# Optimization experiments

Measured on AMD Instinct MI355X. Metric: run time of the kernel, lower is better.

Reference implementation:

```python
import jax, jax.numpy as jnp
import numpy as np

K = 64        # top-k from init_kwargs
TAU = 1.0     # temperature at step=0: tau_start*(1-0) + tau_end*0


def setup_inputs() -> dict:
    key = jax.random.key(0)
    k1, k2 = jax.random.split(key)
    B, N = 2048, 8192
    logits = jax.random.normal(k1, (B, N), dtype=jnp.float32)
    # gumbels = -log(Exp(1)) == standard Gumbel noise
    gumbel_noise = jax.random.gumbel(k2, (B, N), dtype=jnp.float32)
    return {"logits": logits, "gumbel_noise": gumbel_noise}


def reference(logits, gumbel_noise):
    # training path of GumbelTopK (step=0 -> tau=TAU, hard=True)
    g = (logits + gumbel_noise) / TAU                       # [B, N]
    order = jnp.argsort(-g, axis=-1)                        # descending sort order
    sorted_g = jnp.take_along_axis(g, order, axis=-1)
    cumsum = jnp.cumsum(jax.nn.softmax(sorted_g, axis=-1), axis=-1)
    mask = (cumsum <= K).astype(sorted_g.dtype)             # NB: faithful to source (<= k)
    sorted_y = mask * jax.nn.softmax(sorted_g / TAU, axis=-1)
    # scatter back to original positions == gather by inverse permutation
    inv = jnp.argsort(order, axis=-1)
    y = jnp.take_along_axis(sorted_y, inv, axis=-1)         # [B, N]
    # hard straight-through: one-hot-k of y
    k = min(K, y.shape[-1])
    _, idx = jax.lax.top_k(y, k)                            # [B, k]
    rows = jnp.arange(y.shape[0])[:, None]
    y_hard = jnp.zeros_like(y).at[rows, idx].set(1.0)
    return jax.lax.stop_gradient(y_hard - y) + y
```

## Files before the change

kernel.cpp:

```cpp
#include <hip/hip_runtime.h>

constexpr int N = 8192;
constexpr int K = 64;
constexpr int THREADS = 512;
constexpr int WAVES = THREADS / 64;
constexpr int EPT = N / THREADS;
constexpr int VEC = EPT / 4;
constexpr int CAP = 1024;

constexpr float FTHRESH = 4.75f;

typedef float f32x4 __attribute__((ext_vector_type(4)));

__device__ __forceinline__ unsigned orderable(float f) {
    unsigned x = __float_as_uint(f);
    return (x & 0x80000000u) ? ~x : (x | 0x80000000u);
}

__device__ __forceinline__ void barrier_nd() {
    asm volatile("s_waitcnt lgkmcnt(0)" ::: "memory");
    __builtin_amdgcn_s_barrier();
    asm volatile("" ::: "memory");
}

__global__ __launch_bounds__(THREADS, 4)
void gumbel_topk_onehot(const float* __restrict__ logits,
                        const float* __restrict__ noise,
                        float* __restrict__ out)
{
    __shared__ __align__(16) unsigned hist[2048];
    __shared__ __align__(16) unsigned cand[CAP];
    __shared__ unsigned wavesum[WAVES];
    __shared__ unsigned ccount;
    __shared__ unsigned sel_bin, sel_kth, sel_cnt;
    __shared__ unsigned r_val, r_take, r_ceq;

    const int tid  = threadIdx.x;
    const int lane = tid & 63;
    const int wave = tid >> 6;
    const long long row = blockIdx.x;

    if (tid == 0) ccount = 0u;

    const f32x4* l4 = (const f32x4*)(logits + row * (long long)N);
    const f32x4* n4 = (const f32x4*)(noise  + row * (long long)N);
    f32x4 av[VEC], bv[VEC];
#pragma unroll
    for (int i = 0; i < VEC; ++i) av[i] = l4[tid + i * THREADS];
#pragma unroll
    for (int i = 0; i < VEC; ++i) bv[i] = n4[tid + i * THREADS];
#pragma unroll
    for (int i = 0; i < VEC; ++i)
        asm volatile("" : "+v"(av[i]), "+v"(bv[i]));

    float s[EPT];
#pragma unroll
    for (int i = 0; i < VEC; ++i) {
        s[4*i+0] = av[i].x + bv[i].x;
        s[4*i+1] = av[i].y + bv[i].y;
        s[4*i+2] = av[i].z + bv[i].z;
        s[4*i+3] = av[i].w + bv[i].w;
    }
    barrier_nd();

#pragma unroll
    for (int e = 0; e < EPT; ++e) {
        if (s[e] >= FTHRESH) {
            unsigned pos = atomicAdd(&ccount, 1u);
            if (pos < (unsigned)CAP) cand[pos] = __float_as_uint(s[e]);
        }
    }
    barrier_nd();

    const unsigned c = ccount;
    float Tf;
    unsigned take_eq, c_eq;

    if (c >= (unsigned)K && c <= (unsigned)THREADS) {
        const bool have = (tid < (int)c);
        const unsigned myv = have ? cand[tid] : 0u;
        if (tid < (int)((c + 63u) & ~63u)) {
            unsigned g = 0, eq = 0;
            int j = 0;
            for (; j + 4 <= (int)c; j += 4) {
                uint4 v = ((const uint4*)cand)[j >> 2];
                g  += (v.x >  myv) + (v.y >  myv) + (v.z >  myv) + (v.w >  myv);
                eq += (v.x == myv) + (v.y == myv) + (v.z == myv) + (v.w == myv);
            }
            for (; j < (int)c; ++j) {
                unsigned v = cand[j];
                g += (v > myv); eq += (v == myv);
            }
            if (have && g < (unsigned)K && g + eq >= (unsigned)K) {
                r_val  = myv;
                r_take = (unsigned)K - g;
                r_ceq  = eq;
            }
        }
        barrier_nd();
        Tf      = __uint_as_float(r_val);
        take_eq = r_take;
        c_eq    = r_ceq;
    } else {
        unsigned kth = K;

#define SELECT_BIN(BPT)                                                      \
        {                                                                    \
            unsigned p = 0;                                                  \
            _Pragma("unroll")                                                \
            for (int j = 0; j < (BPT); ++j) p += hist[tid * (BPT) + j];      \
            unsigned sc = p;                                                 \
            _Pragma("unroll")                                                \
            for (int off = 1; off < 64; off <<= 1) {                         \
                unsigned v = __shfl_down(sc, off);                           \
                if (lane + off < 64) sc += v;                                \
            }                                                                \
            if (lane == 0) wavesum[wave] = sc;                               \
            __syncthreads();                                                 \
            unsigned S = sc;                                                 \
            _Pragma("unroll")                                                \
            for (int w = 0; w < WAVES; ++w) if (w > wave) S += wavesum[w];   \
            unsigned Snext = S - p;                                          \
            if (S >= kth && Snext < kth) {                                   \
                unsigned cum = Snext;                                        \
                for (int j = (BPT) - 1; j >= 0; --j) {                       \
                    unsigned b = tid * (BPT) + j;                            \
                    unsigned cc = hist[b];                                   \
                    if (cum + cc >= kth) {                                   \
                        sel_bin = b;                                         \
                        sel_kth = kth - cum;                                 \
                        sel_cnt = cc;                                        \
                        break;                                               \
                    }                                                        \
                    cum += cc;                                               \
                }                                                            \
            }                                                                \
            __syncthreads();                                                 \
        }

        ((uint4*)hist)[tid] = make_uint4(0u, 0u, 0u, 0u);
        if (tid == 0) ccount = 0u;
        __syncthreads();
#pragma unroll
        for (int e = 0; e < EPT; ++e)
            atomicAdd(&hist[orderable(s[e]) >> 21], 1u);
        __syncthreads();
        SELECT_BIN(4)
        const unsigned b1   = sel_bin;
        const unsigned cnt1 = sel_cnt;
        kth = sel_kth;

#pragma unroll
        for (int e = 0; e < EPT; ++e) {
            unsigned k_e = orderable(s[e]);
            if ((k_e >> 21) == b1) {
                unsigned pos = atomicAdd(&ccount, 1u);
                if (pos < (unsigned)CAP) cand[pos] = k_e & 0x1FFFFFu;
            }
        }
        __syncthreads();
        const bool use_cand = (cnt1 <= (unsigned)CAP);

        ((uint4*)hist)[tid] = make_uint4(0u, 0u, 0u, 0u);
        __syncthreads();
        if (use_cand) {
            for (int i = tid; i < (int)cnt1; i += THREADS)
                atomicAdd(&hist[cand[i] >> 10], 1u);
        } else {
#pragma unroll
            for (int e = 0; e < EPT; ++e) {
                unsigned k_e = orderable(s[e]);
                if ((k_e >> 21) == b1)
                    atomicAdd(&hist[(k_e >> 10) & 0x7FFu], 1u);
            }
        }
        __syncthreads();
        SELECT_BIN(4)
        const unsigned b2 = sel_bin;
        kth = sel_kth;
        __syncthreads();

        if (tid < 256) ((uint4*)hist)[tid] = make_uint4(0u, 0u, 0u, 0u);
        __syncthreads();
        if (use_cand) {
            for (int i = tid; i < (int)cnt1; i += THREADS) {
                unsigned cv = cand[i];
                if ((cv >> 10) == b2) atomicAdd(&hist[cv & 0x3FFu], 1u);
            }
        } else {
            const unsigned pfx = (b1 << 11) | b2;
#pragma unroll
            for (int e = 0; e < EPT; ++e) {
                unsigned k_e = orderable(s[e]);
                if ((k_e >> 10) == pfx)
                    atomicAdd(&hist[k_e & 0x3FFu], 1u);
            }
        }
        __syncthreads();
        SELECT_BIN(2)
        const unsigned T_ord = (b1 << 21) | (b2 << 10) | sel_bin;
        const unsigned bits = (T_ord & 0x80000000u) ? (T_ord & 0x7FFFFFFFu)
                                                    : ~T_ord;
        Tf      = __uint_as_float(bits);
        take_eq = sel_kth;
        c_eq    = sel_cnt;
#undef SELECT_BIN
    }

    const bool fast = (take_eq == c_eq);

    f32x4* orow = (f32x4*)(out + row * (long long)N);
    if (fast) {
#pragma unroll
        for (int i = 0; i < VEC; ++i) {
            f32x4 o;
            o.x = (s[4*i+0] >= Tf) ? 1.0f : 0.0f;
            o.y = (s[4*i+1] >= Tf) ? 1.0f : 0.0f;
            o.z = (s[4*i+2] >= Tf) ? 1.0f : 0.0f;
            o.w = (s[4*i+3] >= Tf) ? 1.0f : 0.0f;
            __builtin_nontemporal_store(o, &orow[tid + i * THREADS]);
        }
    } else {
#pragma unroll
        for (int i = 0; i < VEC; ++i) {
            f32x4 o;
            o.x = (s[4*i+0] > Tf) ? 1.0f : 0.0f;
            o.y = (s[4*i+1] > Tf) ? 1.0f : 0.0f;
            o.z = (s[4*i+2] > Tf) ? 1.0f : 0.0f;
            o.w = (s[4*i+3] > Tf) ? 1.0f : 0.0f;
            __builtin_nontemporal_store(o, &orow[tid + i * THREADS]);
        }
        __syncthreads();
        if (tid == 0) {
            const float* lf = logits + row * (long long)N;
            const float* nf = noise  + row * (long long)N;
            float* of = out + row * (long long)N;
            unsigned cc = 0;
            for (int i = 0; i < N; ++i) {
                if (lf[i] + nf[i] == Tf) {
                    of[i] = 1.0f;
                    if (++cc == take_eq) break;
                }
            }
        }
    }
}

extern "C" void kernel_launch(void* const* d_in, const int* in_sizes, int n_in,
                              void* d_out, int out_size, void* d_ws, size_t ws_size,
                              hipStream_t stream) {
    const float* logits = (const float*)d_in[0];
    const float* noise  = (const float*)d_in[1];
    float* out = (float*)d_out;
    const int rows = in_sizes[0] / N;
    gumbel_topk_onehot<<<rows, THREADS, 0, stream>>>(logits, noise, out);
}
```

Before: 173.7 us.

## Halve block size, use per-wave ballot compaction instead of shared atomics

Drops the block to 256 threads, so each thread holds 32 elements and more blocks fit per CU. Candidates above the threshold are gathered with ballot and popcount into per-wave segments instead of atomics on one shared counter, and the rank-selection step reads from those segments. Global loads are interleaved in pairs, and nontemporal output stores become ordinary stores. The cost is more register pressure per thread and a fallback to the histogram path when any wave finds more than 64 candidates.

New measurement: 190.4 us. +9.6%, slower.

```diff
diff --git a/kernel.cpp b/kernel.cpp
--- a/kernel.cpp
+++ b/kernel.cpp
@@ -2,10 +2,11 @@
 
 constexpr int N = 8192;
 constexpr int K = 64;
-constexpr int THREADS = 512;
+constexpr int THREADS = 256;
 constexpr int WAVES = THREADS / 64;
 constexpr int EPT = N / THREADS;
 constexpr int VEC = EPT / 4;
+constexpr int SEGCAP = 64;
 constexpr int CAP = 1024;
 
 constexpr float FTHRESH = 4.75f;
@@ -23,13 +24,15 @@
     asm volatile("" ::: "memory");
 }
 
-__global__ __launch_bounds__(THREADS, 4)
+__global__ __launch_bounds__(THREADS, 8)
 void gumbel_topk_onehot(const float* __restrict__ logits,
                         const float* __restrict__ noise,
                         float* __restrict__ out)
 {
     __shared__ __align__(16) unsigned hist[2048];
     __shared__ __align__(16) unsigned cand[CAP];
+    __shared__ __align__(16) unsigned seg[WAVES][SEGCAP];
+    __shared__ unsigned scnt[WAVES];
     __shared__ unsigned wavesum[WAVES];
     __shared__ unsigned ccount;
     __shared__ unsigned sel_bin, sel_kth, sel_cnt;
@@ -40,56 +43,69 @@
     const int wave = tid >> 6;
     const long long row = blockIdx.x;
 
-    if (tid == 0) ccount = 0u;
-
     const f32x4* l4 = (const f32x4*)(logits + row * (long long)N);
     const f32x4* n4 = (const f32x4*)(noise  + row * (long long)N);
-    f32x4 av[VEC], bv[VEC];
-#pragma unroll
-    for (int i = 0; i < VEC; ++i) av[i] = l4[tid + i * THREADS];
-#pragma unroll
-    for (int i = 0; i < VEC; ++i) bv[i] = n4[tid + i * THREADS];
-#pragma unroll
-    for (int i = 0; i < VEC; ++i)
-        asm volatile("" : "+v"(av[i]), "+v"(bv[i]));
-
     float s[EPT];
 #pragma unroll
-    for (int i = 0; i < VEC; ++i) {
-        s[4*i+0] = av[i].x + bv[i].x;
-        s[4*i+1] = av[i].y + bv[i].y;
-        s[4*i+2] = av[i].z + bv[i].z;
-        s[4*i+3] = av[i].w + bv[i].w;
-    }
+    for (int g4 = 0; g4 < VEC; g4 += 2) {
+        f32x4 a0 = l4[tid + (g4 + 0) * THREADS];
+        f32x4 a1 = l4[tid + (g4 + 1) * THREADS];
+        f32x4 b0 = n4[tid + (g4 + 0) * THREADS];
+        f32x4 b1 = n4[tid + (g4 + 1) * THREADS];
+#pragma unroll
+        for (int e = 0; e < 4; ++e) s[4 * g4 + e]     = a0[e] + b0[e];
+#pragma unroll
+        for (int e = 0; e < 4; ++e) s[4 * g4 + 4 + e] = a1[e] + b1[e];
+    }
+
+    const unsigned long long below = (1ull << lane) - 1ull;
+    unsigned cw = 0;
+#pragma unroll
+    for (int e = 0; e < EPT; ++e) {
+        const bool p = (s[e] >= FTHRESH);
+        const unsigned long long m = __ballot(p);
+        if (p) {
+            const unsigned pos = cw + (unsigned)__popcll(m & below);
+            if (pos < (unsigned)SEGCAP) seg[wave][pos] = __float_as_uint(s[e]);
+        }
+        cw += (unsigned)__popcll(m);
+    }
+    if (lane == 0) scnt[wave] = cw;
     barrier_nd();
 
-#pragma unroll
-    for (int e = 0; e < EPT; ++e) {
-        if (s[e] >= FTHRESH) {
-            unsigned pos = atomicAdd(&ccount, 1u);
-            if (pos < (unsigned)CAP) cand[pos] = __float_as_uint(s[e]);
-        }
-    }
-    barrier_nd();
-
-    const unsigned c = ccount;
+    const unsigned c0 = scnt[0], c1 = scnt[1], c2 = scnt[2], c3 = scnt[3];
+    const unsigned c  = c0 + c1 + c2 + c3;
+    const unsigned mx = max(max(c0, c1), max(c2, c3));
+    const unsigned cws[WAVES] = {c0, c1, c2, c3};
+
     float Tf;
     unsigned take_eq, c_eq;
-
-    if (c >= (unsigned)K && c <= (unsigned)THREADS) {
+    bool fast;
+
+    if (c >= (unsigned)K && c <= (unsigned)THREADS && mx <= (unsigned)SEGCAP) {
         const bool have = (tid < (int)c);
-        const unsigned myv = have ? cand[tid] : 0u;
+        unsigned myv = 0u;
+        if (have) {
+            unsigned d = (unsigned)tid, w2 = 0;
+            if (d >= c0) { d -= c0; w2 = 1;
+                if (d >= c1) { d -= c1; w2 = 2;
+                    if (d >= c2) { d -= c2; w2 = 3; } } }
+            myv = seg[w2][d];
+        }
         if (tid < (int)((c + 63u) & ~63u)) {
             unsigned g = 0, eq = 0;
-            int j = 0;
-            for (; j + 4 <= (int)c; j += 4) {
-                uint4 v = ((const uint4*)cand)[j >> 2];
-                g  += (v.x >  myv) + (v.y >  myv) + (v.z >  myv) + (v.w >  myv);
-                eq += (v.x == myv) + (v.y == myv) + (v.z == myv) + (v.w == myv);
-            }
-            for (; j < (int)c; ++j) {
-                unsigned v = cand[j];
-                g += (v > myv); eq += (v == myv);
+#pragma unroll
+            for (int w2 = 0; w2 < WAVES; ++w2) {
+                const unsigned cn = cws[w2];
+                const uint4* s4 = (const uint4*)seg[w2];
+                for (unsigned q = 0; q * 4 < cn; ++q) {
+                    const uint4 v = s4[q];
+                    const unsigned i0 = q * 4;
+                    if (i0 + 0 < cn) { g += v.x > myv; eq += v.x == myv; }
+                    if (i0 + 1 < cn) { g += v.y > myv; eq += v.y == myv; }
+                    if (i0 + 2 < cn) { g += v.z > myv; eq += v.z == myv; }
+                    if (i0 + 3 < cn) { g += v.w > myv; eq += v.w == myv; }
+                }
             }
             if (have && g < (unsigned)K && g + eq >= (unsigned)K) {
                 r_val  = myv;
@@ -101,6 +117,7 @@
         Tf      = __uint_as_float(r_val);
         take_eq = r_take;
         c_eq    = r_ceq;
+        fast    = (take_eq == c_eq);
     } else {
         unsigned kth = K;
 
@@ -138,30 +155,32 @@
             __syncthreads();                                                 \
         }
 
-        ((uint4*)hist)[tid] = make_uint4(0u, 0u, 0u, 0u);
+        for (int i = tid; i < 512; i += THREADS)
+            ((uint4*)hist)[i] = make_uint4(0u, 0u, 0u, 0u);
         if (tid == 0) ccount = 0u;
         __syncthreads();
 #pragma unroll
         for (int e = 0; e < EPT; ++e)
             atomicAdd(&hist[orderable(s[e]) >> 21], 1u);
         __syncthreads();
-        SELECT_BIN(4)
+        SELECT_BIN(8)
         const unsigned b1   = sel_bin;
         const unsigned cnt1 = sel_cnt;
         kth = sel_kth;
 
 #pragma unroll
         for (int e = 0; e < EPT; ++e) {
-            unsigned k_e = orderable(s[e]);
+            const unsigned k_e = orderable(s[e]);
             if ((k_e >> 21) == b1) {
-                unsigned pos = atomicAdd(&ccount, 1u);
+                const unsigned pos = atomicAdd(&ccount, 1u);
                 if (pos < (unsigned)CAP) cand[pos] = k_e & 0x1FFFFFu;
             }
         }
         __syncthreads();
         const bool use_cand = (cnt1 <= (unsigned)CAP);
 
-        ((uint4*)hist)[tid] = make_uint4(0u, 0u, 0u, 0u);
+        for (int i = tid; i < 512; i += THREADS)
+            ((uint4*)hist)[i] = make_uint4(0u, 0u, 0u, 0u);
         __syncthreads();
         if (use_cand) {
             for (int i = tid; i < (int)cnt1; i += THREADS)
@@ -169,45 +188,45 @@
         } else {
 #pragma unroll
             for (int e = 0; e < EPT; ++e) {
-                unsigned k_e = orderable(s[e]);
+                const unsigned k_e = orderable(s[e]);
                 if ((k_e >> 21) == b1)
                     atomicAdd(&hist[(k_e >> 10) & 0x7FFu], 1u);
             }
         }
         __syncthreads();
-        SELECT_BIN(4)
+        SELECT_BIN(8)
         const unsigned b2 = sel_bin;
         kth = sel_kth;
         __syncthreads();
 
-        if (tid < 256) ((uint4*)hist)[tid] = make_uint4(0u, 0u, 0u, 0u);
+        for (int i = tid; i < 256; i += THREADS)
+            ((uint4*)hist)[i] = make_uint4(0u, 0u, 0u, 0u);
         __syncthreads();
         if (use_cand) {
             for (int i = tid; i < (int)cnt1; i += THREADS) {
-                unsigned cv = cand[i];
+                const unsigned cv = cand[i];
                 if ((cv >> 10) == b2) atomicAdd(&hist[cv & 0x3FFu], 1u);
             }
         } else {
             const unsigned pfx = (b1 << 11) | b2;
 #pragma unroll
             for (int e = 0; e < EPT; ++e) {
-                unsigned k_e = orderable(s[e]);
+                const unsigned k_e = orderable(s[e]);
                 if ((k_e >> 10) == pfx)
                     atomicAdd(&hist[k_e & 0x3FFu], 1u);
             }
         }
         __syncthreads();
-        SELECT_BIN(2)
+        SELECT_BIN(4)
         const unsigned T_ord = (b1 << 21) | (b2 << 10) | sel_bin;
         const unsigned bits = (T_ord & 0x80000000u) ? (T_ord & 0x7FFFFFFFu)
                                                     : ~T_ord;
         Tf      = __uint_as_float(bits);
         take_eq = sel_kth;
         c_eq    = sel_cnt;
+        fast    = (take_eq == c_eq);
 #undef SELECT_BIN
     }
-
-    const bool fast = (take_eq == c_eq);
 
     f32x4* orow = (f32x4*)(out + row * (long long)N);
     if (fast) {
@@ -218,7 +237,7 @@
             o.y = (s[4*i+1] >= Tf) ? 1.0f : 0.0f;
             o.z = (s[4*i+2] >= Tf) ? 1.0f : 0.0f;
             o.w = (s[4*i+3] >= Tf) ? 1.0f : 0.0f;
-            __builtin_nontemporal_store(o, &orow[tid + i * THREADS]);
+            orow[tid + i * THREADS] = o;
         }
     } else {
 #pragma unroll
@@ -228,7 +247,7 @@
             o.y = (s[4*i+1] > Tf) ? 1.0f : 0.0f;
             o.z = (s[4*i+2] > Tf) ? 1.0f : 0.0f;
             o.w = (s[4*i+3] > Tf) ? 1.0f : 0.0f;
-            __builtin_nontemporal_store(o, &orow[tid + i * THREADS]);
+            orow[tid + i * THREADS] = o;
         }
         __syncthreads();
         if (tid == 0) {
```
